# Optimization experiments

Measured on AMD Instinct MI355X. Metric: run time of the kernel, lower is better.

## Reference

```python
import jax, jax.numpy as jnp
import numpy as np

SIZE = 512
HEADS = 4
DK = SIZE // HEADS
CHUNK = 16
SHIFT = 8
EPS = 1e-12


def layer_norm(x, g, b):
    m = jnp.mean(x, axis=-1, keepdims=True)
    v = jnp.var(x, axis=-1, keepdims=True)
    return (x - m) / jnp.sqrt(v + EPS) * g + b


def setup_inputs() -> dict:
    key = jax.random.key(0)
    ks = jax.random.split(key, 8)
    B, L, C = 16, 2048, SIZE
    p = lambda k, shp: jax.random.normal(k, shp, jnp.float32) * 0.02
    return {
        "x": jax.random.normal(ks[0], (B, L, C), jnp.float32),
        "mask": jnp.ones((B, 1, L), jnp.float32),
        "pos_emb": jnp.zeros((1, L, C), jnp.float32),
        "mask_pad": jnp.ones((B, 1, L), jnp.float32),
        "Wq": p(ks[1], (C, C)), "bq": jnp.zeros((C,), jnp.float32),
        "Wk": p(ks[2], (C, C)), "bk": jnp.zeros((C,), jnp.float32),
        "Wv": p(ks[3], (C, C)), "bv": jnp.zeros((C,), jnp.float32),
        "Wo": p(ks[4], (C, C)), "bo": jnp.zeros((C,), jnp.float32),
        "g1": jnp.ones((C,), jnp.float32), "be1": jnp.zeros((C,), jnp.float32),
        "g2": jnp.ones((C,), jnp.float32), "be2": jnp.zeros((C,), jnp.float32),
        "W1": p(ks[5], (C, 4 * C)), "bf1": jnp.zeros((4 * C,), jnp.float32),
        "W2": p(ks[6], (4 * C, C)), "bf2": jnp.zeros((C,), jnp.float32),
    }


def reference(x, mask, pos_emb, mask_pad, Wq, bq, Wk, bk, Wv, bv, Wo, bo,
              g1, be1, g2, be2, W1, bf1, W2, bf2):
    B, L, C = x.shape
    nW = L // CHUNK
    half = CHUNK // 2
    # shifted-window attention mask, built exactly as in the torch code
    # (zeros base, -100 in the cross-shift blocks); shape (nW, CHUNK, CHUNK)
    am = jnp.zeros((nW, CHUNK, CHUNK), x.dtype)
    am = am.at[:-1, :half - 1, half:].set(-100.0)
    am = am.at[-1, half:, half:].set(-100.0)

    residual = x
    xn = layer_norm(x, g1, be1)  # normalize_before

    # cyclic shift
    sx = jnp.roll(xn, -SHIFT, axis=1)                    # (B, L, C)
    sm = jnp.roll(mask_pad[:, 0, :], -SHIFT, axis=1)     # (B, L)

    # chunk partition
    xc = sx.reshape(B, nW, CHUNK, C)
    mc = sm.reshape(B, nW, CHUNK)

    # windowed multi-head attention
    q = (xc @ Wq + bq).reshape(B, nW, CHUNK, HEADS, DK)
    k = (xc @ Wk + bk).reshape(B, nW, CHUNK, HEADS, DK)
    v = (xc @ Wv + bv).reshape(B, nW, CHUNK, HEADS, DK)
    scores = jnp.einsum('bwqhd,bwkhd->bwhqk', q, k) / jnp.sqrt(jnp.asarray(DK, x.dtype))
    scores = scores + am[None, :, None]                  # add shift mask per chunk
    valid = mc[:, :, None, None, :] > 0.0                # key padding mask
    scores = jnp.where(valid, scores, jnp.asarray(-1e30, x.dtype))
    attn = jax.nn.softmax(scores, axis=-1)
    attn = jnp.where(valid, attn, jnp.asarray(0.0, x.dtype))
    out = jnp.einsum('bwhqk,bwkhd->bwqhd', attn, v).reshape(B, nW, CHUNK, C)
    out = out @ Wo + bo

    # chunk reverse + reverse shift
    sx_out = out.reshape(B, L, C)
    xa = jnp.roll(sx_out, SHIFT, axis=1)
    m = jnp.roll(sm, SHIFT, axis=1)
    xa = xa * m[:, :, None]
    x1 = residual + xa  # dropout_rate = 0

    # feed forward block (pre-norm, ReLU FFN)
    residual2 = x1
    xn2 = layer_norm(x1, g2, be2)
    h = jax.nn.relu(xn2 @ W1 + bf1)
    x2 = residual2 + (h @ W2 + bf2)
    return x2
```

## Files before the change

kernel.cpp:

```cpp
#include <hip/hip_runtime.h>
#include <stdint.h>


typedef unsigned short bfu;

using bf16x8 = __attribute__((ext_vector_type(8))) __bf16;
using f32x4  = __attribute__((ext_vector_type(4))) float;

union U8 { uint4 v; unsigned short s[8]; };
union F4 { float4 v; float f[4]; };
union ABFrag { uint4 u; bf16x8 f; };

__device__ __forceinline__ float bf2f(unsigned short u) {
    union { uint32_t i; float f; } c; c.i = ((uint32_t)u) << 16; return c.f;
}
__device__ __forceinline__ unsigned short f2bf(float f) {
    union { float f; uint32_t i; } c; c.f = f;
    uint32_t x = c.i;
    return (unsigned short)((x + 0x7FFFu + ((x >> 16) & 1u)) >> 16);
}
__device__ __forceinline__ uint4 pack8(float4 a, float4 b) {
    U8 o;
    o.s[0] = f2bf(a.x); o.s[1] = f2bf(a.y); o.s[2] = f2bf(a.z); o.s[3] = f2bf(a.w);
    o.s[4] = f2bf(b.x); o.s[5] = f2bf(b.y); o.s[6] = f2bf(b.z); o.s[7] = f2bf(b.w);
    return o.v;
}

#define GLDS16(gp, lp)                                                        \
    __builtin_amdgcn_global_load_lds(                                         \
        (__attribute__((address_space(1))) void*)(gp),                        \
        (__attribute__((address_space(3))) void*)(lp), 16, 0, 0)


__global__ __launch_bounds__(256) void wconv_kernel(
    const float* __restrict__ W, bfu* __restrict__ Wt, int K, int N)
{
    __shared__ float t[32][33];
    const int bn = blockIdx.x << 5;
    const int bk = blockIdx.y << 5;
    const int tx = threadIdx.x & 31, ty = threadIdx.x >> 5;
#pragma unroll
    for (int i = 0; i < 32; i += 8)
        t[ty + i][tx] = W[(size_t)(bk + ty + i) * N + bn + tx];
    __syncthreads();
#pragma unroll
    for (int i = 0; i < 32; i += 8)
        Wt[(size_t)(bn + ty + i) * K + bk + tx] = f2bf(t[tx][ty + i]);
}

__global__ __launch_bounds__(256) void bias_concat_kernel(
    const float* __restrict__ a, const float* __restrict__ b,
    const float* __restrict__ c, float* __restrict__ o)
{
    const int t = blockIdx.x * 256 + threadIdx.x;
    const float* src = (t < 512) ? a : (t < 1024) ? b : c;
    o[t] = src[t & 511];
}


__global__ __launch_bounds__(64) void ln1_shift_kernel(
    const float* __restrict__ x, const float* __restrict__ g,
    const float* __restrict__ be, bfu* __restrict__ out)
{
    const int ms = blockIdx.x;
    const int b = ms >> 11;
    const int ls = ms & 2047;
    const int l = (ls + 8) & 2047;
    const int c0 = threadIdx.x << 3;
    const float* xp = x + ((((size_t)(b << 11)) + l) << 9) + c0;
    F4 f0, f1; f0.v = *(const float4*)xp; f1.v = *(const float4*)(xp + 4);
    float vv[8]; float s = 0.f, sq = 0.f;
#pragma unroll
    for (int j = 0; j < 4; ++j) { vv[j] = f0.f[j]; vv[4 + j] = f1.f[j]; }
#pragma unroll
    for (int j = 0; j < 8; ++j) { s += vv[j]; sq += vv[j] * vv[j]; }
#pragma unroll
    for (int o = 32; o > 0; o >>= 1) { s += __shfl_xor(s, o); sq += __shfl_xor(sq, o); }
    const float mean = s * (1.f / 512.f);
    float var = sq * (1.f / 512.f) - mean * mean;
    var = fmaxf(var, 0.f);
    const float rstd = rsqrtf(var + 1e-12f);
    F4 g0, g1v, b0, b1;
    g0.v = *(const float4*)(g + c0);  g1v.v = *(const float4*)(g + c0 + 4);
    b0.v = *(const float4*)(be + c0); b1.v = *(const float4*)(be + c0 + 4);
    U8 o8;
#pragma unroll
    for (int j = 0; j < 4; ++j) {
        o8.s[j]     = f2bf((vv[j]     - mean) * rstd * g0.f[j]  + b0.f[j]);
        o8.s[4 + j] = f2bf((vv[4 + j] - mean) * rstd * g1v.f[j] + b1.f[j]);
    }
    *(uint4*)(out + (((size_t)ms) << 9) + c0) = o8.v;
}

__global__ __launch_bounds__(64) void ln2_kernel(
    const bfu* __restrict__ x1, const float* __restrict__ g,
    const float* __restrict__ be, bfu* __restrict__ out)
{
    const int ms = blockIdx.x;
    const int c0 = threadIdx.x << 3;
    U8 u; u.v = *(const uint4*)(x1 + (((size_t)ms) << 9) + c0);
    float vv[8]; float s = 0.f, sq = 0.f;
#pragma unroll
    for (int j = 0; j < 8; ++j) { float f = bf2f(u.s[j]); vv[j] = f; s += f; sq += f * f; }
#pragma unroll
    for (int o = 32; o > 0; o >>= 1) { s += __shfl_xor(s, o); sq += __shfl_xor(sq, o); }
    const float mean = s * (1.f / 512.f);
    float var = sq * (1.f / 512.f) - mean * mean;
    var = fmaxf(var, 0.f);
    const float rstd = rsqrtf(var + 1e-12f);
    F4 g0, g1v, b0, b1;
    g0.v = *(const float4*)(g + c0);  g1v.v = *(const float4*)(g + c0 + 4);
    b0.v = *(const float4*)(be + c0); b1.v = *(const float4*)(be + c0 + 4);
    U8 o8;
#pragma unroll
    for (int j = 0; j < 4; ++j) {
        o8.s[j]     = f2bf((vv[j]     - mean) * rstd * g0.f[j]  + b0.f[j]);
        o8.s[4 + j] = f2bf((vv[4 + j] - mean) * rstd * g1v.f[j] + b1.f[j]);
    }
    *(uint4*)(out + (((size_t)ms) << 9) + c0) = o8.v;
}


template<int EPI>
__global__ __launch_bounds__(512) void mgemm(
    const bfu* __restrict__ X, const bfu* __restrict__ Wt,
    const float* __restrict__ bias,
    bfu* Ob, float* Ofl,
    const float* __restrict__ xres, const bfu* __restrict__ prevb,
    const float* __restrict__ maskpad,
    int M, int N, int K)
{
    __shared__ __align__(16) char smem[131072];
    bfu* smb = (bfu*)smem;
    const char* smc = (const char*)smem;
    float* epi = (float*)smem;

    const int t = threadIdx.x;
    const int lane = t & 63;
    const int w = t >> 6;
    const int wm = w >> 2, wn = w & 3;
    const int q = lane >> 4, l15 = lane & 15;

    const int gx = gridDim.x;
    const int nwg = gx * gridDim.y;
    int wid = blockIdx.y * gx + blockIdx.x;
    wid = ((wid & 7) * (nwg >> 3)) + (wid >> 3);
    const int row0 = (wid / gx) << 8;
    const int col0 = (wid % gx) << 8;

    const int srow = (w << 3) + (lane >> 3);
    const int scol = (((lane & 7) ^ ((lane >> 3) & 7)) << 3);
    const bfu* gA = X  + (size_t)(row0 + srow) * K + scol;
    const bfu* gB = Wt + (size_t)(col0 + srow) * K + scol;
    bfu* lsA0 = smb + (w << 9) + (lane << 3);
    bfu* lsB0 = lsA0 + 16384;
    bfu* lsA1 = lsA0 + 32768;
    bfu* lsB1 = lsA0 + 49152;

    const int arow = ((wm << 7) + l15) << 7;
    const int brow = ((wn << 6) + l15) << 7;
    const int qb   = q << 4;
    const int swz  = (l15 & 7) << 4;

    f32x4 acc[8][4];
    float bv[4];
#pragma unroll
    for (int j = 0; j < 4; ++j) bv[j] = bias[col0 + (wn << 6) + (j << 4) + l15];
#pragma unroll
    for (int i = 0; i < 8; ++i)
#pragma unroll
        for (int j = 0; j < 4; ++j) {
            acc[i][j][0] = bv[j]; acc[i][j][1] = bv[j];
            acc[i][j][2] = bv[j]; acc[i][j][3] = bv[j];
        }

    ABFrag a[4][2];
    ABFrag bb[2][2][2];

#define SCHB_ __builtin_amdgcn_sched_barrier(0)
#define SB_   do { __builtin_amdgcn_s_barrier(); SCHB_; } while (0)
#define LGKM0_ do { asm volatile("s_waitcnt lgkmcnt(0)" ::: "memory"); SCHB_; } while (0)
#define VM8_   do { asm volatile("s_waitcnt vmcnt(8)" ::: "memory"); SCHB_; } while (0)
#define VM0_   do { asm volatile("s_waitcnt vmcnt(0)" ::: "memory"); SCHB_; } while (0)

#define LDA_(D, MH)                                                           \
    _Pragma("unroll") for (int mf = 0; mf < 4; ++mf)                          \
    _Pragma("unroll") for (int kk = 0; kk < 2; ++kk)                          \
        a[mf][kk].u = *(const uint4*)(smc + (D)*65536 + arow + (MH)*8192 +    \
                                      mf*2048 + (((kk << 6) + qb) ^ swz));
#define LDB_(D, NH)                                                           \
    _Pragma("unroll") for (int nf = 0; nf < 2; ++nf)                          \
    _Pragma("unroll") for (int kk = 0; kk < 2; ++kk)                          \
        bb[NH][nf][kk].u = *(const uint4*)(smc + (D)*65536 + 32768 + brow +   \
                                      (NH)*4096 + nf*2048 +                   \
                                      (((kk << 6) + qb) ^ swz));
#define MFMAQ_(MH, NH)                                                        \
    __builtin_amdgcn_s_setprio(1);                                            \
    _Pragma("unroll") for (int mf = 0; mf < 4; ++mf)                          \
    _Pragma("unroll") for (int nf = 0; nf < 2; ++nf) {                        \
        acc[(MH)*4+mf][(NH)*2+nf] = __builtin_amdgcn_mfma_f32_16x16x32_bf16(  \
            a[mf][0].f, bb[NH][nf][0].f, acc[(MH)*4+mf][(NH)*2+nf], 0, 0, 0); \
        acc[(MH)*4+mf][(NH)*2+nf] = __builtin_amdgcn_mfma_f32_16x16x32_bf16(  \
            a[mf][1].f, bb[NH][nf][1].f, acc[(MH)*4+mf][(NH)*2+nf], 0, 0, 0);}\
    __builtin_amdgcn_s_setprio(0);
#define STGA4_(D, GA2) do {                                                   \
    GLDS16((GA2), lsA##D);                                                    \
    GLDS16((GA2) + (size_t)64  * K, lsA##D + 4096);                           \
    GLDS16((GA2) + (size_t)128 * K, lsA##D + 8192);                           \
    GLDS16((GA2) + (size_t)192 * K, lsA##D + 12288); } while (0)
#define STGB4_(D, GB2) do {                                                   \
    GLDS16((GB2), lsB##D);                                                    \
    GLDS16((GB2) + (size_t)64  * K, lsB##D + 4096);                           \
    GLDS16((GB2) + (size_t)128 * K, lsB##D + 8192);                           \
    GLDS16((GB2) + (size_t)192 * K, lsB##D + 12288); } while (0)
#define TILE_(D, DOSTG, GA2, GB2, VMW) do {                                   \
    LDA_(D, 0); LDB_(D, 0);                                                   \
    SB_; LGKM0_; MFMAQ_(0, 0); SB_;                                           \
    LDB_(D, 1);                                                               \
    SB_; LGKM0_; MFMAQ_(0, 1); SB_;                                           \
    LDA_(D, 1);                                                               \
    if (DOSTG) { SCHB_; STGB4_(D, GB2); }                                     \
    SB_; LGKM0_; MFMAQ_(1, 0); SB_;                                           \
    if (DOSTG) { STGA4_(D, GA2); SCHB_; }                                     \
    SB_; LGKM0_; MFMAQ_(1, 1);                                                \
    VMW;                                                                      \
    SB_; } while (0)

    const int nT = K >> 6;

    STGA4_(0, gA); STGB4_(0, gB);
    SCHB_;
    {
        const bfu* ga1 = gA + 64; const bfu* gb1 = gB + 64;
        STGA4_(1, ga1); STGB4_(1, gb1);
    }
    SCHB_;
    VM8_;
    SB_;

    const bfu* gA2 = gA + 128;
    const bfu* gB2 = gB + 128;
#pragma unroll 1
    for (int tt = 0; tt < nT - 2; tt += 2) {
        TILE_(0, true, gA2, gB2, VM8_);
        gA2 += 64; gB2 += 64;
        TILE_(1, true, gA2, gB2, VM8_);
        gA2 += 64; gB2 += 64;
    }
    TILE_(0, false, gA2, gB2, VM0_);
    TILE_(1, false, gA2, gB2, (void)0);

#undef LDA_
#undef LDB_
#undef MFMAQ_
#undef STGA4_
#undef STGB4_
#undef TILE_

    float* epw = epi + w * 1088;
    const int c8 = (lane & 7) << 3;
    const int r8 = lane >> 3;
    const int colg = col0 + (wn << 6) + c8;
#pragma unroll
    for (int i = 0; i < 8; ++i) {
#pragma unroll
        for (int j = 0; j < 4; ++j)
#pragma unroll
            for (int r = 0; r < 4; ++r) {
                float y = acc[i][j][r];
                if (EPI == 1) y = fmaxf(y, 0.f);
                epw[((q << 2) + r) * 68 + (j << 4) + l15] = y;
            }
        __builtin_amdgcn_wave_barrier();
#pragma unroll
        for (int h = 0; h < 2; ++h) {
            const int rr = r8 + (h << 3);
            F4 f0, f1;
            f0.v = *(const float4*)&epw[rr * 68 + c8];
            f1.v = *(const float4*)&epw[rr * 68 + c8 + 4];
            const int row_out = row0 + (wm << 7) + (i << 4) + rr;
            if (EPI == 0 || EPI == 1) {
                *(uint4*)(Ob + (size_t)row_out * N + colg) = pack8(f0.v, f1.v);
            } else if (EPI == 2) {
                const int bb2 = row_out >> 11;
                const int ls = row_out & 2047;
                const int l = (ls + 8) & 2047;
                const float mp = maskpad[(bb2 << 11) + l];
                const size_t dst = ((size_t)(bb2 << 11) + l) * (size_t)N + colg;
                F4 x0, x1v;
                x0.v = *(const float4*)(xres + dst);
                x1v.v = *(const float4*)(xres + dst + 4);
                F4 o0, o1;
#pragma unroll
                for (int jj = 0; jj < 4; ++jj) {
                    o0.f[jj] = x0.f[jj]  + f0.f[jj] * mp;
                    o1.f[jj] = x1v.f[jj] + f1.f[jj] * mp;
                }
                *(uint4*)(Ob + dst) = pack8(o0.v, o1.v);
            } else {
                const size_t dst = (size_t)row_out * N + colg;
                U8 pb; pb.v = *(const uint4*)(prevb + dst);
                F4 o0, o1;
#pragma unroll
                for (int jj = 0; jj < 4; ++jj) {
                    o0.f[jj] = bf2f(pb.s[jj])     + f0.f[jj];
                    o1.f[jj] = bf2f(pb.s[4 + jj]) + f1.f[jj];
                }
                *(float4*)(Ofl + dst) = o0.v;
                *(float4*)(Ofl + dst + 4) = o1.v;
            }
        }
        __builtin_amdgcn_wave_barrier();
    }
}


__global__ __launch_bounds__(256) void attn_kernel(
    const bfu* __restrict__ qkv, const float* __restrict__ mpad,
    bfu* __restrict__ out)
{
    __shared__ float qs[16][129];
    __shared__ float ks[16][129];
    __shared__ float vs[16][129];
    __shared__ float ps[16][17];
    const int t = threadIdx.x;
    const int wg = blockIdx.x;
    const int h = blockIdx.y;
    const int b = wg >> 7;
    const int w = wg & 127;
    const int li = t >> 4;
    const int d0 = (t & 15) << 3;
    const size_t bi = (((size_t)wg << 4) + li) * 1536 + (h << 7) + d0;
    U8 uq, uk, uv;
    uq.v = *(const uint4*)(qkv + bi);
    uk.v = *(const uint4*)(qkv + bi + 512);
    uv.v = *(const uint4*)(qkv + bi + 1024);
#pragma unroll
    for (int j = 0; j < 8; ++j) {
        qs[li][d0 + j] = bf2f(uq.s[j]);
        ks[li][d0 + j] = bf2f(uk.s[j]);
        vs[li][d0 + j] = bf2f(uv.s[j]);
    }
    __syncthreads();
    const int qi = li, ki = t & 15;
    float s = 0.f;
#pragma unroll 8
    for (int d = 0; d < 128; ++d) s += qs[qi][d] * ks[ki][d];
    s *= 0.088388347648318447f;
    const bool lastw = (w == 127);
    if (lastw ? (qi >= 8 && ki >= 8) : (qi < 7 && ki >= 8)) s -= 100.f;
    const int lkey = ((w << 4) + ki + 8) & 2047;
    const bool valid = mpad[(b << 11) + lkey] > 0.f;
    if (!valid) s = -1e30f;
    float mx = s;
#pragma unroll
    for (int o = 8; o > 0; o >>= 1) mx = fmaxf(mx, __shfl_xor(mx, o, 16));
    float e = __expf(s - mx);
    float sum = e;
#pragma unroll
    for (int o = 8; o > 0; o >>= 1) sum += __shfl_xor(sum, o, 16);
    float p = e / sum;
    if (!valid) p = 0.f;
    ps[qi][ki] = p;
    __syncthreads();
    float o_[8];
#pragma unroll
    for (int j = 0; j < 8; ++j) o_[j] = 0.f;
#pragma unroll
    for (int kk = 0; kk < 16; ++kk) {
        const float pw = ps[li][kk];
#pragma unroll
        for (int j = 0; j < 8; ++j) o_[j] += pw * vs[kk][d0 + j];
    }
    U8 o8;
#pragma unroll
    for (int j = 0; j < 8; ++j) o8.s[j] = f2bf(o_[j]);
    *(uint4*)(out + (((size_t)wg << 4) + li) * 512 + (h << 7) + d0) = o8.v;
}


extern "C" void kernel_launch(void* const* d_in, const int* in_sizes, int n_in,
                              void* d_out, int out_size, void* d_ws, size_t ws_size,
                              hipStream_t stream)
{
    const float* x    = (const float*)d_in[0];
    const float* mpad = (const float*)d_in[3];
    const float* Wq = (const float*)d_in[4];  const float* bq = (const float*)d_in[5];
    const float* Wk = (const float*)d_in[6];  const float* bk = (const float*)d_in[7];
    const float* Wv = (const float*)d_in[8];  const float* bv = (const float*)d_in[9];
    const float* Wo = (const float*)d_in[10]; const float* bo = (const float*)d_in[11];
    const float* g1 = (const float*)d_in[12]; const float* be1 = (const float*)d_in[13];
    const float* g2 = (const float*)d_in[14]; const float* be2 = (const float*)d_in[15];
    const float* W1 = (const float*)d_in[16]; const float* bf1 = (const float*)d_in[17];
    const float* W2 = (const float*)d_in[18]; const float* bf2 = (const float*)d_in[19];
    float* out = (float*)d_out;

    char* p = (char*)d_ws;
    const size_t MB = (size_t)1 << 20;
    bfu* xn_s = (bfu*)p;
    bfu* att  = xn_s;
    bfu* qkv  = (bfu*)(p + 32 * MB);
    bfu* x1   = qkv;
    bfu* W1t  = (bfu*)(p + 64 * MB);
    bfu* W2t  = (bfu*)(p + 66 * MB);
    bfu* xn2  = (bfu*)(p + 96 * MB);
    bfu* hreg = (bfu*)(p + 128 * MB);
    bfu* Wqkvt = hreg;
    bfu* Wot   = hreg + 1536 * 512;
    float* bqkv = (float*)(hreg + 2048 * 512);

    const int M = 32768;
    dim3 blk(256);
    dim3 blk5(512);

    wconv_kernel<<<dim3(16, 16), blk, 0, stream>>>(Wq, Wqkvt, 512, 512);
    wconv_kernel<<<dim3(16, 16), blk, 0, stream>>>(Wk, Wqkvt + 512 * 512, 512, 512);
    wconv_kernel<<<dim3(16, 16), blk, 0, stream>>>(Wv, Wqkvt + 1024 * 512, 512, 512);
    wconv_kernel<<<dim3(16, 16), blk, 0, stream>>>(Wo, Wot, 512, 512);
    bias_concat_kernel<<<dim3(6), blk, 0, stream>>>(bq, bk, bv, bqkv);

    ln1_shift_kernel<<<32768, 64, 0, stream>>>(x, g1, be1, xn_s);

    mgemm<0><<<dim3(6, 128), blk5, 0, stream>>>(xn_s, Wqkvt, bqkv, qkv, nullptr, nullptr, nullptr, nullptr, M, 1536, 512);

    attn_kernel<<<dim3(2048, 4), blk, 0, stream>>>(qkv, mpad, att);

    wconv_kernel<<<dim3(64, 16), blk, 0, stream>>>(W1, W1t, 512, 2048);
    wconv_kernel<<<dim3(16, 64), blk, 0, stream>>>(W2, W2t, 2048, 512);

    mgemm<2><<<dim3(2, 128), blk5, 0, stream>>>(att, Wot, bo, x1, nullptr, x, nullptr, mpad, M, 512, 512);

    ln2_kernel<<<32768, 64, 0, stream>>>(x1, g2, be2, xn2);

    mgemm<1><<<dim3(8, 128), blk5, 0, stream>>>(xn2, W1t, bf1, hreg, nullptr, nullptr, nullptr, nullptr, M, 2048, 512);
    mgemm<3><<<dim3(2, 128), blk5, 0, stream>>>(hreg, W2t, bf2, nullptr, out, nullptr, x1, nullptr, M, 512, 2048);
}
```

Baseline: 554.1 us.

## Software-pipeline LDS fragment loads across MFMA quadrants with double A registers

Restructures the GEMM main loop so each LDS fragment load for the next quadrant, and for the next tile's first A and B fragments, is issued before the current quadrant's MFMAs run. It uses two A register sets and removes the explicit lgkmcnt(0) waits and sched_barriers, leaving the compiler to insert waits. The global-load wait moves to vmcnt(4) with a different staging order. This aims to hide LDS latency behind matrix math. In exchange it raises register pressure and relies on barrier placement being correct for the double-buffered LDS.

Measured after the change: 997.8 us. 1.8x slower.

```diff
diff --git a/kernel.cpp b/kernel.cpp
--- a/kernel.cpp
+++ b/kernel.cpp
@@ -174,19 +174,25 @@
             acc[i][j][2] = bv[j]; acc[i][j][3] = bv[j];
         }
 
-    ABFrag a[4][2];
+    ABFrag aA[4][2];
+    ABFrag aB[4][2];
     ABFrag bb[2][2][2];
 
-#define SCHB_ __builtin_amdgcn_sched_barrier(0)
-#define SB_   do { __builtin_amdgcn_s_barrier(); SCHB_; } while (0)
-#define LGKM0_ do { asm volatile("s_waitcnt lgkmcnt(0)" ::: "memory"); SCHB_; } while (0)
-#define VM8_   do { asm volatile("s_waitcnt vmcnt(8)" ::: "memory"); SCHB_; } while (0)
-#define VM0_   do { asm volatile("s_waitcnt vmcnt(0)" ::: "memory"); SCHB_; } while (0)
-
-#define LDA_(D, MH)                                                           \
-    _Pragma("unroll") for (int mf = 0; mf < 4; ++mf)                          \
+#define SB_   __builtin_amdgcn_s_barrier()
+#define VM8_  asm volatile("s_waitcnt vmcnt(8)" ::: "memory")
+#define VM4_  asm volatile("s_waitcnt vmcnt(4)" ::: "memory")
+#define VM0_  asm volatile("s_waitcnt vmcnt(0)" ::: "memory")
+#define VMNOP_ do {} while (0)
+
+#define LDAA_(D, M0, M1)                                                      \
+    _Pragma("unroll") for (int mf = (M0); mf <= (M1); ++mf)                   \
     _Pragma("unroll") for (int kk = 0; kk < 2; ++kk)                          \
-        a[mf][kk].u = *(const uint4*)(smc + (D)*65536 + arow + (MH)*8192 +    \
+        aA[mf][kk].u = *(const uint4*)(smc + (D)*65536 + arow +               \
+                                      mf*2048 + (((kk << 6) + qb) ^ swz));
+#define LDAB_(D, M0, M1)                                                      \
+    _Pragma("unroll") for (int mf = (M0); mf <= (M1); ++mf)                   \
+    _Pragma("unroll") for (int kk = 0; kk < 2; ++kk)                          \
+        aB[mf][kk].u = *(const uint4*)(smc + (D)*65536 + arow + 8192 +        \
                                       mf*2048 + (((kk << 6) + qb) ^ swz));
 #define LDB_(D, NH)                                                           \
     _Pragma("unroll") for (int nf = 0; nf < 2; ++nf)                          \
@@ -194,14 +200,14 @@
         bb[NH][nf][kk].u = *(const uint4*)(smc + (D)*65536 + 32768 + brow +   \
                                       (NH)*4096 + nf*2048 +                   \
                                       (((kk << 6) + qb) ^ swz));
-#define MFMAQ_(MH, NH)                                                        \
+#define MFMAQ_(AR, MH, NH)                                                    \
     __builtin_amdgcn_s_setprio(1);                                            \
     _Pragma("unroll") for (int mf = 0; mf < 4; ++mf)                          \
     _Pragma("unroll") for (int nf = 0; nf < 2; ++nf) {                        \
         acc[(MH)*4+mf][(NH)*2+nf] = __builtin_amdgcn_mfma_f32_16x16x32_bf16(  \
-            a[mf][0].f, bb[NH][nf][0].f, acc[(MH)*4+mf][(NH)*2+nf], 0, 0, 0); \
+            AR[mf][0].f, bb[NH][nf][0].f, acc[(MH)*4+mf][(NH)*2+nf], 0,0,0);  \
         acc[(MH)*4+mf][(NH)*2+nf] = __builtin_amdgcn_mfma_f32_16x16x32_bf16(  \
-            a[mf][1].f, bb[NH][nf][1].f, acc[(MH)*4+mf][(NH)*2+nf], 0, 0, 0);}\
+            AR[mf][1].f, bb[NH][nf][1].f, acc[(MH)*4+mf][(NH)*2+nf], 0,0,0);} \
     __builtin_amdgcn_s_setprio(0);
 #define STGA4_(D, GA2) do {                                                   \
     GLDS16((GA2), lsA##D);                                                    \
@@ -213,49 +219,57 @@
     GLDS16((GB2) + (size_t)64  * K, lsB##D + 4096);                           \
     GLDS16((GB2) + (size_t)128 * K, lsB##D + 8192);                           \
     GLDS16((GB2) + (size_t)192 * K, lsB##D + 12288); } while (0)
-#define TILE_(D, DOSTG, GA2, GB2, VMW) do {                                   \
-    LDA_(D, 0); LDB_(D, 0);                                                   \
-    SB_; LGKM0_; MFMAQ_(0, 0); SB_;                                           \
-    LDB_(D, 1);                                                               \
-    SB_; LGKM0_; MFMAQ_(0, 1); SB_;                                           \
-    LDA_(D, 1);                                                               \
-    if (DOSTG) { SCHB_; STGB4_(D, GB2); }                                     \
-    SB_; LGKM0_; MFMAQ_(1, 0); SB_;                                           \
-    if (DOSTG) { STGA4_(D, GA2); SCHB_; }                                     \
-    SB_; LGKM0_; MFMAQ_(1, 1);                                                \
+
+#define TILE_(D, DOSTG, LASTT, VMW) do {                                      \
+    SB_;                                                                      \
+    LDB_(D, 1); LDAB_(D, 0, 1);                                               \
+    MFMAQ_(aA, 0, 0);                                                         \
+    SB_;                                                                      \
+    LDAB_(D, 2, 3);                                                           \
+    if (DOSTG) STGB4_(D, gB2);                                                \
+    MFMAQ_(aA, 0, 1);                                                         \
     VMW;                                                                      \
-    SB_; } while (0)
+    SB_;                                                                      \
+    if (!(LASTT)) { LDAA_((D)^1, 0, 1); }                                     \
+    if (DOSTG) STGA4_(D, gA2);                                                \
+    MFMAQ_(aB, 1, 0);                                                         \
+    SB_;                                                                      \
+    if (!(LASTT)) { LDAA_((D)^1, 2, 3); LDB_((D)^1, 0); }                     \
+    MFMAQ_(aB, 1, 1);                                                         \
+} while (0)
 
     const int nT = K >> 6;
 
     STGA4_(0, gA); STGB4_(0, gB);
-    SCHB_;
     {
         const bfu* ga1 = gA + 64; const bfu* gb1 = gB + 64;
         STGA4_(1, ga1); STGB4_(1, gb1);
     }
-    SCHB_;
     VM8_;
     SB_;
+    LDAA_(0, 0, 3); LDB_(0, 0);
 
     const bfu* gA2 = gA + 128;
     const bfu* gB2 = gB + 128;
 #pragma unroll 1
     for (int tt = 0; tt < nT - 2; tt += 2) {
-        TILE_(0, true, gA2, gB2, VM8_);
+        TILE_(0, true, false, VM4_);
         gA2 += 64; gB2 += 64;
-        TILE_(1, true, gA2, gB2, VM8_);
+        TILE_(1, true, false, VM4_);
         gA2 += 64; gB2 += 64;
     }
-    TILE_(0, false, gA2, gB2, VM0_);
-    TILE_(1, false, gA2, gB2, (void)0);
-
-#undef LDA_
+    TILE_(0, false, false, VM0_);
+    TILE_(1, false, true,  VMNOP_);
+
+#undef LDAA_
+#undef LDAB_
 #undef LDB_
 #undef MFMAQ_
 #undef STGA4_
 #undef STGB4_
 #undef TILE_
+
+    SB_;
 
     float* epw = epi + w * 1088;
     const int c8 = (lane & 7) << 3;
```
